# Optimization experiments

Measured on AMD Instinct MI355X. Metric: run time of the kernel, lower is better.

The kernel has to match this reference:

```python
import jax, jax.numpy as jnp
import numpy as np

B, L, DIM = 4, 8192, 512
HEADS, WIN = 8, 256
HID = int(DIM * 4.0)
HEAD_DIM = DIM // HEADS
EPS = 1e-5


def _layernorm(x, g, b):
    m = jnp.mean(x, axis=-1, keepdims=True)
    v = jnp.mean(jnp.square(x - m), axis=-1, keepdims=True)
    return (x - m) * jax.lax.rsqrt(v + EPS) * g + b


def setup_inputs() -> dict:
    key = jax.random.key(0)
    ks = jax.random.split(key, 8)
    s = 0.02
    return {
        "x": jax.random.normal(ks[0], (B, L, DIM), jnp.float32),
        "norm1_g": jnp.ones((DIM,), jnp.float32),
        "norm1_b": jnp.zeros((DIM,), jnp.float32),
        "qkv_w": jax.random.normal(ks[1], (DIM, 3 * DIM), jnp.float32) * s,
        "qkv_b": jnp.zeros((3 * DIM,), jnp.float32),
        "rpb_table": jax.random.normal(ks[2], (2 * WIN - 1, HEADS), jnp.float32) * s,
        "proj_w": jax.random.normal(ks[3], (DIM, DIM), jnp.float32) * s,
        "proj_b": jnp.zeros((DIM,), jnp.float32),
        "norm2_g": jnp.ones((DIM,), jnp.float32),
        "norm2_b": jnp.zeros((DIM,), jnp.float32),
        "fc1_w": jax.random.normal(ks[4], (DIM, HID), jnp.float32) * s,
        "fc1_b": jnp.zeros((HID,), jnp.float32),
        "fc2_w": jax.random.normal(ks[5], (HID, DIM), jnp.float32) * s,
        "fc2_b": jnp.zeros((DIM,), jnp.float32),
    }


def reference(x, norm1_g, norm1_b, qkv_w, qkv_b, rpb_table, proj_w, proj_b,
              norm2_g, norm2_b, fc1_w, fc1_b, fc2_w, fc2_b):
    scale = HEAD_DIM ** -0.5
    nW = L // WIN
    BW = B * nW

    shortcut = x
    h = _layernorm(x, norm1_g, norm1_b)
    xw = h.reshape(BW, WIN, DIM)

    qkv = (xw @ qkv_w + qkv_b).reshape(BW, WIN, 3, HEADS, HEAD_DIM)
    q = jnp.moveaxis(qkv[:, :, 0], 1, 2) * scale  # (BW, H, W, d)
    k = jnp.moveaxis(qkv[:, :, 1], 1, 2)
    v = jnp.moveaxis(qkv[:, :, 2], 1, 2)

    attn = jnp.einsum('bhqd,bhkd->bhqk', q, k)
    # relative position bias gather: (W, W, H) -> (H, W, W)
    coords = jnp.arange(WIN)
    ridx = coords[:, None] - coords[None, :] + WIN - 1
    bias = rpb_table[ridx]  # (W, W, H)
    attn = attn + jnp.transpose(bias, (2, 0, 1))[None]
    attn = jax.nn.softmax(attn, axis=-1)

    out = jnp.einsum('bhqk,bhkd->bhqd', attn, v)  # (BW, H, W, d)
    out = jnp.moveaxis(out, 1, 2).reshape(BW, WIN, DIM)
    out = out @ proj_w + proj_b

    x = shortcut + out.reshape(B, L, DIM)
    # NOTE: norm2 output feeds BOTH the residual branch and the MLP (as in source)
    x = _layernorm(x, norm2_g, norm2_b)
    m = jax.nn.gelu(x @ fc1_w + fc1_b, approximate=False) @ fc2_w + fc2_b
    return x + m
```

## Files before the change

kernel.cpp:

```cpp
#include <hip/hip_runtime.h>
#include <hip/hip_bf16.h>
#include <math.h>
#include <stdint.h>


typedef __attribute__((ext_vector_type(8))) __bf16 bf16x8;
typedef __attribute__((ext_vector_type(4))) __bf16 bf16x4;
typedef __attribute__((ext_vector_type(4))) float  f32x4;

#define NTOK  32768
#define DIMC  512
#define HEADS 8
#define WIN   256
#define HD    64
#define HIDC  2048

__device__ __forceinline__ void gld16(const __bf16* g, __bf16* l)
{
    __builtin_amdgcn_global_load_lds(
        (const __attribute__((address_space(1))) void*)g,
        (__attribute__((address_space(3))) void*)l, 16, 0, 0);
}

#define DSR(dst, base, off) \
    asm volatile("ds_read_b128 %0, %1 offset:" off : "=v"(dst) : "v"(base))

template<int MODE, int OUTF>
__global__ __launch_bounds__(512, 2) void gemm256(
    const __bf16* __restrict__ A, int lda,
    const __bf16* __restrict__ Bt, int ldb,
    const float* __restrict__ bias,
    const void* __restrict__ res, int res_f32,
    void* __restrict__ C, int ldc, int K,
    int nM, int nN)
{
    __shared__ __bf16 lds[2][2][16384];
    const int tid  = threadIdx.x;
    const int wave = tid >> 6, lane = tid & 63;
    const int quad = lane >> 4, l16 = lane & 15;
    const int wm = wave >> 2, wn = wave & 3;

    const int id  = blockIdx.x;
    const int xcd = id & 7;
    const int lid = id >> 3;
    const int mq  = lid / nN;
    const int mt  = xcd * (nM >> 3) + mq;
    const int nt  = lid - mq * nN;
    const int m0 = mt * 256, n0 = nt * 256;

    int aoff[4], boff[4];
    #pragma unroll
    for (int j = 0; j < 4; j++) {
        const int S = wave * 4 + j;
        const int row = (S >> 1) * 16 + l16;
        const int kof = (S & 1) * 32 + quad * 8;
        aoff[j] = (m0 + row) * lda + kof;
        boff[j] = (n0 + row) * ldb + kof;
    }

    const uint32_t lds0 =
        (uint32_t)(uintptr_t)(__attribute__((address_space(3))) void*)&lds[0][0][0];
    const uint32_t aAd0 = lds0 + wm * 16384 + lane * 16;
    const uint32_t bAd0 = lds0 + 32768 + wn * 8192 + lane * 16;

    f32x4 acc[8][4] = {};
    bf16x8 rA[4][2], rB[4][2];

    const int ntk = K >> 6;

    #pragma unroll
    for (int j = 0; j < 4; j++) {
        gld16(A  + aoff[j], &lds[0][0][(wave * 4 + j) * 512]);
        gld16(Bt + boff[j], &lds[0][1][(wave * 4 + j) * 512]);
    }
    #pragma unroll
    for (int j = 0; j < 4; j++) {
        gld16(A  + aoff[j] + 64, &lds[1][0][(wave * 4 + j) * 512]);
        gld16(Bt + boff[j] + 64, &lds[1][1][(wave * 4 + j) * 512]);
    }
    asm volatile("s_waitcnt vmcnt(8)");
    __builtin_amdgcn_s_barrier();

    for (int t = 0; t < ntk; ++t) {
        const int buf = t & 1;
        const uint32_t aAd = aAd0 + buf * 65536;
        const uint32_t bAd = bAd0 + buf * 65536;
        const bool pf = (t + 2 < ntk);
        const int kn = (t + 2) << 6;

        DSR(rA[0][0], aAd, "0");    DSR(rA[0][1], aAd, "1024");
        DSR(rA[1][0], aAd, "2048"); DSR(rA[1][1], aAd, "3072");
        DSR(rA[2][0], aAd, "4096"); DSR(rA[2][1], aAd, "5120");
        DSR(rA[3][0], aAd, "6144"); DSR(rA[3][1], aAd, "7168");
        DSR(rB[0][0], bAd, "0");    DSR(rB[0][1], bAd, "1024");
        DSR(rB[1][0], bAd, "2048"); DSR(rB[1][1], bAd, "3072");
        __builtin_amdgcn_s_barrier();
        asm volatile("s_waitcnt lgkmcnt(0)");
        __builtin_amdgcn_sched_barrier(0);
        __builtin_amdgcn_s_setprio(1);
        #pragma unroll
        for (int i = 0; i < 4; i++)
            #pragma unroll
            for (int j = 0; j < 2; j++)
                #pragma unroll
                for (int ks = 0; ks < 2; ks++)
                    acc[i][j] = __builtin_amdgcn_mfma_f32_16x16x32_bf16(
                        rB[j][ks], rA[i][ks], acc[i][j], 0, 0, 0);
        __builtin_amdgcn_s_setprio(0);
        __builtin_amdgcn_s_barrier();

        DSR(rB[2][0], bAd, "4096"); DSR(rB[2][1], bAd, "5120");
        DSR(rB[3][0], bAd, "6144"); DSR(rB[3][1], bAd, "7168");
        __builtin_amdgcn_s_barrier();
        asm volatile("s_waitcnt lgkmcnt(0)");
        __builtin_amdgcn_sched_barrier(0);
        __builtin_amdgcn_s_setprio(1);
        #pragma unroll
        for (int i = 0; i < 4; i++)
            #pragma unroll
            for (int j = 2; j < 4; j++)
                #pragma unroll
                for (int ks = 0; ks < 2; ks++)
                    acc[i][j] = __builtin_amdgcn_mfma_f32_16x16x32_bf16(
                        rB[j][ks], rA[i][ks], acc[i][j], 0, 0, 0);
        __builtin_amdgcn_s_setprio(0);
        __builtin_amdgcn_s_barrier();

        DSR(rA[0][0], aAd, "8192");  DSR(rA[0][1], aAd, "9216");
        DSR(rA[1][0], aAd, "10240"); DSR(rA[1][1], aAd, "11264");
        DSR(rA[2][0], aAd, "12288"); DSR(rA[2][1], aAd, "13312");
        DSR(rA[3][0], aAd, "14336"); DSR(rA[3][1], aAd, "15360");
        if (pf) {
            #pragma unroll
            for (int j = 0; j < 4; j++)
                gld16(Bt + boff[j] + kn, &lds[buf][1][(wave * 4 + j) * 512]);
        }
        __builtin_amdgcn_s_barrier();
        asm volatile("s_waitcnt lgkmcnt(0)");
        __builtin_amdgcn_sched_barrier(0);
        __builtin_amdgcn_s_setprio(1);
        #pragma unroll
        for (int i = 0; i < 4; i++)
            #pragma unroll
            for (int j = 0; j < 2; j++)
                #pragma unroll
                for (int ks = 0; ks < 2; ks++)
                    acc[4 + i][j] = __builtin_amdgcn_mfma_f32_16x16x32_bf16(
                        rB[j][ks], rA[i][ks], acc[4 + i][j], 0, 0, 0);
        __builtin_amdgcn_s_setprio(0);
        __builtin_amdgcn_s_barrier();

        if (pf) {
            #pragma unroll
            for (int j = 0; j < 4; j++)
                gld16(A + aoff[j] + kn, &lds[buf][0][(wave * 4 + j) * 512]);
        }
        __builtin_amdgcn_s_setprio(1);
        #pragma unroll
        for (int i = 0; i < 4; i++)
            #pragma unroll
            for (int j = 2; j < 4; j++)
                #pragma unroll
                for (int ks = 0; ks < 2; ks++)
                    acc[4 + i][j] = __builtin_amdgcn_mfma_f32_16x16x32_bf16(
                        rB[j][ks], rA[i][ks], acc[4 + i][j], 0, 0, 0);
        __builtin_amdgcn_s_setprio(0);
        if (pf)                  asm volatile("s_waitcnt vmcnt(8)");
        else if (t + 1 < ntk)    asm volatile("s_waitcnt vmcnt(0)");
        __builtin_amdgcn_s_barrier();
    }

    #pragma unroll
    for (int i = 0; i < 8; i++) {
        const int row = m0 + wm * 128 + i * 16 + l16;
        #pragma unroll
        for (int j = 0; j < 4; j++) {
            const int colb = n0 + wn * 64 + j * 16 + quad * 4;
            const size_t off = (size_t)row * ldc + colb;
            const f32x4 bv = *(const f32x4*)(bias + colb);
            f32x4 v;
            #pragma unroll
            for (int r = 0; r < 4; r++) v[r] = acc[i][j][r] + bv[r];
            if (MODE == 2) {
                #pragma unroll
                for (int r = 0; r < 4; r++)
                    v[r] = 0.5f * v[r] * (1.0f + erff(v[r] * 0.70710678118654752f));
            }
            if (MODE == 1) {
                if (res_f32) {
                    const f32x4 rv = *(const f32x4*)((const float*)res + off);
                    #pragma unroll
                    for (int r = 0; r < 4; r++) v[r] += rv[r];
                } else {
                    const bf16x4 rv = *(const bf16x4*)((const __bf16*)res + off);
                    #pragma unroll
                    for (int r = 0; r < 4; r++) v[r] += (float)rv[r];
                }
            }
            if (OUTF) {
                *(f32x4*)((float*)C + off) = v;
            } else {
                bf16x4 o;
                #pragma unroll
                for (int r = 0; r < 4; r++) o[r] = (__bf16)v[r];
                *(bf16x4*)((__bf16*)C + off) = o;
            }
        }
    }
}

__global__ __launch_bounds__(256) void attn_fused(
    const __bf16* __restrict__ qkvb, const float* __restrict__ rpb,
    const __bf16* __restrict__ Vt, __bf16* __restrict__ attnO)
{
    __shared__ __align__(16) __bf16 Ks[256 * 72];
    __shared__ float rpbs[320];
    const int bh = blockIdx.y;
    const int bw = bh >> 3, head = bh & 7;
    const int m0 = blockIdx.x * 64;
    const int tid = threadIdx.x;
    const __bf16* qb = qkvb + (size_t)bw * WIN * 1536 + head * HD;

    const int wave = tid >> 6, lane = tid & 63;
    const int quad = lane >> 4, l16 = lane & 15;

    bf16x8 af[2];
    #pragma unroll
    for (int ks = 0; ks < 2; ks++)
        af[ks] = *(const bf16x8*)(qb + (size_t)(m0 + wave * 16 + l16) * 1536
                                  + ks * 32 + quad * 8);

    {
        const int row = tid >> 3, l8 = (tid & 7) * 8;
        #pragma unroll
        for (int p = 0; p < 8; p++) {
            const int r = p * 32 + row;
            *(bf16x8*)(Ks + r * 72 + l8) =
                *(const bf16x8*)(qb + 512 + (size_t)r * 1536 + l8);
        }
        rpbs[tid] = rpb[(size_t)(m0 + tid) * HEADS + head];
        if (tid < 63) rpbs[256 + tid] = rpb[(size_t)(m0 + 256 + tid) * HEADS + head];
    }
    __syncthreads();

    f32x4 acc[16];
    #pragma unroll
    for (int nb = 0; nb < 16; nb++) acc[nb] = (f32x4){0.f, 0.f, 0.f, 0.f};
    #pragma unroll
    for (int nb = 0; nb < 16; nb++) {
        #pragma unroll
        for (int ks = 0; ks < 2; ks++) {
            bf16x8 bf = *(const bf16x8*)(Ks + (nb * 16 + l16) * 72 + ks * 32 + quad * 8);
            acc[nb] = __builtin_amdgcn_mfma_f32_16x16x32_bf16(bf, af[ks], acc[nb], 0, 0, 0);
        }
    }
    const int ql = wave * 16 + l16;
    #pragma unroll
    for (int nb = 0; nb < 16; nb++)
        #pragma unroll
        for (int r = 0; r < 4; r++)
            acc[nb][r] = acc[nb][r] * 0.125f
                       + rpbs[ql - (nb * 16 + quad * 4 + r) + 255];

    __syncthreads();

    char* Pb = (char*)Ks;
    {
        float m = -1e30f;
        #pragma unroll
        for (int nb = 0; nb < 16; nb++)
            #pragma unroll
            for (int r = 0; r < 4; r++) m = fmaxf(m, acc[nb][r]);
        m = fmaxf(m, __shfl_xor(m, 16));
        m = fmaxf(m, __shfl_xor(m, 32));
        float s = 0.f;
        #pragma unroll
        for (int nb = 0; nb < 16; nb++)
            #pragma unroll
            for (int r = 0; r < 4; r++) {
                acc[nb][r] = __expf(acc[nb][r] - m);
                s += acc[nb][r];
            }
        s += __shfl_xor(s, 16);
        s += __shfl_xor(s, 32);
        const float inv = 1.0f / s;
        const int rx = ql & 7;
        #pragma unroll
        for (int nb = 0; nb < 16; nb++) {
            bf16x4 o;
            #pragma unroll
            for (int r = 0; r < 4; r++) o[r] = (__bf16)(acc[nb][r] * inv);
            const int c = nb * 2 + (quad >> 1);
            *(bf16x4*)(Pb + ql * 512 + ((c ^ rx) << 4) + ((quad & 1) << 3)) = o;
        }
    }
    __syncthreads();

    const __bf16* Vtb = Vt + (size_t)bh * (HD * WIN);
    const int prow = wave * 16 + l16;
    const int px = prow & 7;
    f32x4 acc2[4] = {};
    #pragma unroll
    for (int ks2 = 0; ks2 < 8; ks2++) {
        const bf16x8 pa = *(const bf16x8*)(Pb + prow * 512
                                + (((ks2 * 4 + quad) ^ px) << 4));
        #pragma unroll
        for (int nb2 = 0; nb2 < 4; nb2++) {
            const bf16x8 vf = *(const bf16x8*)(Vtb + (size_t)(nb2 * 16 + l16) * WIN
                                + ks2 * 32 + quad * 8);
            acc2[nb2] = __builtin_amdgcn_mfma_f32_16x16x32_bf16(vf, pa, acc2[nb2], 0, 0, 0);
        }
    }
    {
        const int i = m0 + wave * 16 + l16;
        __bf16* ob = attnO + (size_t)(bw * WIN + i) * DIMC + head * HD;
        #pragma unroll
        for (int nb2 = 0; nb2 < 4; nb2++) {
            bf16x4 o;
            #pragma unroll
            for (int r = 0; r < 4; r++) o[r] = (__bf16)acc2[nb2][r];
            *(bf16x4*)(ob + nb2 * 16 + quad * 4) = o;
        }
    }
}

__global__ __launch_bounds__(256) void vtrans(
    const __bf16* __restrict__ qkvb, __bf16* __restrict__ Vt, int bh_base)
{
    __shared__ __align__(16) __bf16 s[WIN * 72];
    const int bh = bh_base + blockIdx.x;
    const int bw = bh >> 3, head = bh & 7;
    const int tid = threadIdx.x;
    const __bf16* V = qkvb + (size_t)bw * WIN * 1536 + 1024 + head * HD;
    #pragma unroll
    for (int it = 0; it < 8; it++) {
        int idx = it * 256 + tid;
        int j = idx >> 3;
        int d0 = (idx & 7) * 8;
        *(bf16x8*)(s + j * 72 + d0) = *(const bf16x8*)(V + (size_t)j * 1536 + d0);
    }
    __syncthreads();
    __bf16* out = Vt + (size_t)blockIdx.x * (HD * WIN);
    #pragma unroll
    for (int it = 0; it < 8; it++) {
        int idx = it * 256 + tid;
        int d  = idx >> 5;
        int j0 = (idx & 31) * 8;
        bf16x8 v;
        #pragma unroll
        for (int j = 0; j < 8; j++) v[j] = s[(j0 + j) * 72 + d];
        *(bf16x8*)(out + (size_t)d * WIN + j0) = v;
    }
}

__global__ __launch_bounds__(256) void ln_kernel(
    const void* X, int xf,
    const float* __restrict__ g, const float* __restrict__ b,
    __bf16* O)
{
    const int tok  = blockIdx.x * 4 + (threadIdx.x >> 6);
    const int lane = threadIdx.x & 63;
    const size_t base = (size_t)tok * DIMC + lane * 8;
    float v[8];
    if (xf) {
        const float* xp = (const float*)X + base;
        f32x4 a = *(const f32x4*)xp;
        f32x4 c = *(const f32x4*)(xp + 4);
        #pragma unroll
        for (int j = 0; j < 4; j++) { v[j] = a[j]; v[4 + j] = c[j]; }
    } else {
        bf16x8 xv = *(const bf16x8*)((const __bf16*)X + base);
        #pragma unroll
        for (int j = 0; j < 8; j++) v[j] = (float)xv[j];
    }
    float s = 0.f, s2 = 0.f;
    #pragma unroll
    for (int j = 0; j < 8; j++) { s += v[j]; s2 += v[j] * v[j]; }
    #pragma unroll
    for (int off = 32; off; off >>= 1) { s += __shfl_xor(s, off); s2 += __shfl_xor(s2, off); }
    const float mean = s * (1.0f / DIMC);
    const float var  = s2 * (1.0f / DIMC) - mean * mean;
    const float rstd = rsqrtf(var + 1e-5f);
    f32x4 ga = *(const f32x4*)(g + lane * 8);
    f32x4 gc = *(const f32x4*)(g + lane * 8 + 4);
    f32x4 ba = *(const f32x4*)(b + lane * 8);
    f32x4 bc = *(const f32x4*)(b + lane * 8 + 4);
    bf16x8 ov;
    #pragma unroll
    for (int j = 0; j < 4; j++) {
        ov[j]     = (__bf16)((v[j]     - mean) * rstd * ga[j] + ba[j]);
        ov[4 + j] = (__bf16)((v[4 + j] - mean) * rstd * gc[j] + bc[j]);
    }
    *(bf16x8*)(O + base) = ov;
}

__global__ __launch_bounds__(256) void wtrans(
    const float* __restrict__ W, __bf16* __restrict__ Wt, int K, int N)
{
    __shared__ __align__(16) __bf16 s[64 * 72];
    const int kb = blockIdx.y * 64, nb = blockIdx.x * 64;
    const int tid = threadIdx.x;
    #pragma unroll
    for (int it = 0; it < 2; it++) {
        int idx = it * 256 + tid;
        int lk = idx >> 3;
        int ln = (idx & 7) * 8;
        const float* wp = W + (size_t)(kb + lk) * N + nb + ln;
        f32x4 a = *(const f32x4*)wp;
        f32x4 c = *(const f32x4*)(wp + 4);
        bf16x8 v;
        #pragma unroll
        for (int j = 0; j < 4; j++) { v[j] = (__bf16)a[j]; v[4 + j] = (__bf16)c[j]; }
        *(bf16x8*)(s + lk * 72 + ln) = v;
    }
    __syncthreads();
    #pragma unroll
    for (int it = 0; it < 2; it++) {
        int idx = it * 256 + tid;
        int ln  = idx >> 3;
        int lkv = (idx & 7) * 8;
        bf16x8 v;
        #pragma unroll
        for (int j = 0; j < 8; j++) v[j] = s[(lkv + j) * 72 + ln];
        *(bf16x8*)(Wt + (size_t)(nb + ln) * K + kb + lkv) = v;
    }
}

extern "C" void kernel_launch(void* const* d_in, const int* in_sizes, int n_in,
                              void* d_out, int out_size, void* d_ws, size_t ws_size,
                              hipStream_t stream)
{
    const float* x      = (const float*)d_in[0];
    const float* n1g    = (const float*)d_in[1];
    const float* n1b    = (const float*)d_in[2];
    const float* qkv_w  = (const float*)d_in[3];
    const float* qkv_b  = (const float*)d_in[4];
    const float* rpb    = (const float*)d_in[5];
    const float* proj_w = (const float*)d_in[6];
    const float* proj_b = (const float*)d_in[7];
    const float* n2g    = (const float*)d_in[8];
    const float* n2b    = (const float*)d_in[9];
    const float* fc1_w  = (const float*)d_in[10];
    const float* fc1_b  = (const float*)d_in[11];
    const float* fc2_w  = (const float*)d_in[12];
    const float* fc2_b  = (const float*)d_in[13];
    float* out = (float*)d_out;

    char* ws = (char*)d_ws;
    __bf16* qkvb  = (__bf16*)(ws + 0);
    __bf16* hid   = (__bf16*)(ws + 0);
    __bf16* Vt    = (__bf16*)(ws + 100663296);
    __bf16* h     = (__bf16*)(ws + 134217728);
    __bf16* y     = h;
    __bf16* attnO = (__bf16*)(ws + 167772160);
    __bf16* wq_t  = (__bf16*)(ws + 209715200);
    __bf16* wp_t  = (__bf16*)(ws + 211288064);
    __bf16* w1_t  = (__bf16*)(ws + 211812352);
    __bf16* w2_t  = (__bf16*)(ws + 213909504);

    wtrans<<<dim3(1536 / 64, 512 / 64),  256, 0, stream>>>(qkv_w, wq_t, 512, 1536);
    wtrans<<<dim3(512 / 64,  512 / 64),  256, 0, stream>>>(proj_w, wp_t, 512, 512);
    wtrans<<<dim3(2048 / 64, 512 / 64),  256, 0, stream>>>(fc1_w, w1_t, 512, 2048);
    wtrans<<<dim3(512 / 64,  2048 / 64), 256, 0, stream>>>(fc2_w, w2_t, 2048, 512);

    ln_kernel<<<NTOK / 4, 256, 0, stream>>>(x, 1, n1g, n1b, h);

    gemm256<0, 0><<<768, 512, 0, stream>>>(
        h, DIMC, wq_t, DIMC, qkv_b, nullptr, 0, qkvb, 1536, DIMC, 128, 6);

    vtrans<<<1024, 256, 0, stream>>>(qkvb, Vt, 0);
    attn_fused<<<dim3(4, 1024), 256, 0, stream>>>(qkvb, rpb, Vt, attnO);

    gemm256<1, 0><<<256, 512, 0, stream>>>(
        attnO, DIMC, wp_t, DIMC, proj_b, x, 1, y, DIMC, DIMC, 128, 2);

    ln_kernel<<<NTOK / 4, 256, 0, stream>>>(y, 0, n2g, n2b, y);

    gemm256<2, 0><<<1024, 512, 0, stream>>>(
        y, DIMC, w1_t, DIMC, fc1_b, nullptr, 0, hid, HIDC, DIMC, 128, 8);

    gemm256<1, 1><<<256, 512, 0, stream>>>(
        hid, HIDC, w2_t, HIDC, fc2_b, y, 0, out, DIMC, HIDC, 128, 2);
}
```

Before: 634.0 us.

## Replace 256x256 double-buffered GEMM with 128x128 single-buffered 4-wave tile

```diff
diff --git a/kernel.cpp b/kernel.cpp
--- a/kernel.cpp
+++ b/kernel.cpp
@@ -26,7 +26,7 @@
     asm volatile("ds_read_b128 %0, %1 offset:" off : "=v"(dst) : "v"(base))
 
 template<int MODE, int OUTF>
-__global__ __launch_bounds__(512, 2) void gemm256(
+__global__ __launch_bounds__(256, 3) void gemm128m(
     const __bf16* __restrict__ A, int lda,
     const __bf16* __restrict__ Bt, int ldb,
     const float* __restrict__ bias,
@@ -34,11 +34,11 @@
     void* __restrict__ C, int ldc, int K,
     int nM, int nN)
 {
-    __shared__ __bf16 lds[2][2][16384];
+    __shared__ __bf16 lds[16384];
     const int tid  = threadIdx.x;
     const int wave = tid >> 6, lane = tid & 63;
     const int quad = lane >> 4, l16 = lane & 15;
-    const int wm = wave >> 2, wn = wave & 3;
+    const int wr = wave >> 1, wc = wave & 1;
 
     const int id  = blockIdx.x;
     const int xcd = id & 7;
@@ -46,7 +46,7 @@
     const int mq  = lid / nN;
     const int mt  = xcd * (nM >> 3) + mq;
     const int nt  = lid - mq * nN;
-    const int m0 = mt * 256, n0 = nt * 256;
+    const int m0 = mt * 128, n0 = nt * 128;
 
     int aoff[4], boff[4];
     #pragma unroll
@@ -59,123 +59,66 @@
     }
 
     const uint32_t lds0 =
-        (uint32_t)(uintptr_t)(__attribute__((address_space(3))) void*)&lds[0][0][0];
-    const uint32_t aAd0 = lds0 + wm * 16384 + lane * 16;
-    const uint32_t bAd0 = lds0 + 32768 + wn * 8192 + lane * 16;
-
-    f32x4 acc[8][4] = {};
+        (uint32_t)(uintptr_t)(__attribute__((address_space(3))) void*)&lds[0];
+    const uint32_t aAd = lds0 + wr * 8192 + lane * 16;
+    const uint32_t bAd = lds0 + 16384 + wc * 8192 + lane * 16;
+
+    f32x4 acc[4][4] = {};
     bf16x8 rA[4][2], rB[4][2];
 
     const int ntk = K >> 6;
 
     #pragma unroll
     for (int j = 0; j < 4; j++) {
-        gld16(A  + aoff[j], &lds[0][0][(wave * 4 + j) * 512]);
-        gld16(Bt + boff[j], &lds[0][1][(wave * 4 + j) * 512]);
-    }
-    #pragma unroll
-    for (int j = 0; j < 4; j++) {
-        gld16(A  + aoff[j] + 64, &lds[1][0][(wave * 4 + j) * 512]);
-        gld16(Bt + boff[j] + 64, &lds[1][1][(wave * 4 + j) * 512]);
-    }
-    asm volatile("s_waitcnt vmcnt(8)");
+        gld16(A  + aoff[j], &lds[(wave * 4 + j) * 512]);
+        gld16(Bt + boff[j], &lds[8192 + (wave * 4 + j) * 512]);
+    }
+    asm volatile("s_waitcnt vmcnt(0)");
     __builtin_amdgcn_s_barrier();
 
     for (int t = 0; t < ntk; ++t) {
-        const int buf = t & 1;
-        const uint32_t aAd = aAd0 + buf * 65536;
-        const uint32_t bAd = bAd0 + buf * 65536;
-        const bool pf = (t + 2 < ntk);
-        const int kn = (t + 2) << 6;
-
         DSR(rA[0][0], aAd, "0");    DSR(rA[0][1], aAd, "1024");
         DSR(rA[1][0], aAd, "2048"); DSR(rA[1][1], aAd, "3072");
         DSR(rA[2][0], aAd, "4096"); DSR(rA[2][1], aAd, "5120");
         DSR(rA[3][0], aAd, "6144"); DSR(rA[3][1], aAd, "7168");
         DSR(rB[0][0], bAd, "0");    DSR(rB[0][1], bAd, "1024");
         DSR(rB[1][0], bAd, "2048"); DSR(rB[1][1], bAd, "3072");
-        __builtin_amdgcn_s_barrier();
+        DSR(rB[2][0], bAd, "4096"); DSR(rB[2][1], bAd, "5120");
+        DSR(rB[3][0], bAd, "6144"); DSR(rB[3][1], bAd, "7168");
         asm volatile("s_waitcnt lgkmcnt(0)");
         __builtin_amdgcn_sched_barrier(0);
+        __builtin_amdgcn_s_barrier();
+
+        const bool pf = (t + 1 < ntk);
+        if (pf) {
+            const int kn = (t + 1) << 6;
+            #pragma unroll
+            for (int j = 0; j < 4; j++) {
+                gld16(A  + aoff[j] + kn, &lds[(wave * 4 + j) * 512]);
+                gld16(Bt + boff[j] + kn, &lds[8192 + (wave * 4 + j) * 512]);
+            }
+        }
+
         __builtin_amdgcn_s_setprio(1);
         #pragma unroll
         for (int i = 0; i < 4; i++)
             #pragma unroll
-            for (int j = 0; j < 2; j++)
+            for (int j = 0; j < 4; j++)
                 #pragma unroll
                 for (int ks = 0; ks < 2; ks++)
                     acc[i][j] = __builtin_amdgcn_mfma_f32_16x16x32_bf16(
                         rB[j][ks], rA[i][ks], acc[i][j], 0, 0, 0);
         __builtin_amdgcn_s_setprio(0);
+        if (pf) asm volatile("s_waitcnt vmcnt(0)");
         __builtin_amdgcn_s_barrier();
-
-        DSR(rB[2][0], bAd, "4096"); DSR(rB[2][1], bAd, "5120");
-        DSR(rB[3][0], bAd, "6144"); DSR(rB[3][1], bAd, "7168");
-        __builtin_amdgcn_s_barrier();
-        asm volatile("s_waitcnt lgkmcnt(0)");
-        __builtin_amdgcn_sched_barrier(0);
-        __builtin_amdgcn_s_setprio(1);
-        #pragma unroll
-        for (int i = 0; i < 4; i++)
-            #pragma unroll
-            for (int j = 2; j < 4; j++)
-                #pragma unroll
-                for (int ks = 0; ks < 2; ks++)
-                    acc[i][j] = __builtin_amdgcn_mfma_f32_16x16x32_bf16(
-                        rB[j][ks], rA[i][ks], acc[i][j], 0, 0, 0);
-        __builtin_amdgcn_s_setprio(0);
-        __builtin_amdgcn_s_barrier();
-
-        DSR(rA[0][0], aAd, "8192");  DSR(rA[0][1], aAd, "9216");
-        DSR(rA[1][0], aAd, "10240"); DSR(rA[1][1], aAd, "11264");
-        DSR(rA[2][0], aAd, "12288"); DSR(rA[2][1], aAd, "13312");
-        DSR(rA[3][0], aAd, "14336"); DSR(rA[3][1], aAd, "15360");
-        if (pf) {
-            #pragma unroll
-            for (int j = 0; j < 4; j++)
-                gld16(Bt + boff[j] + kn, &lds[buf][1][(wave * 4 + j) * 512]);
-        }
-        __builtin_amdgcn_s_barrier();
-        asm volatile("s_waitcnt lgkmcnt(0)");
-        __builtin_amdgcn_sched_barrier(0);
-        __builtin_amdgcn_s_setprio(1);
-        #pragma unroll
-        for (int i = 0; i < 4; i++)
-            #pragma unroll
-            for (int j = 0; j < 2; j++)
-                #pragma unroll
-                for (int ks = 0; ks < 2; ks++)
-                    acc[4 + i][j] = __builtin_amdgcn_mfma_f32_16x16x32_bf16(
-                        rB[j][ks], rA[i][ks], acc[4 + i][j], 0, 0, 0);
-        __builtin_amdgcn_s_setprio(0);
-        __builtin_amdgcn_s_barrier();
-
-        if (pf) {
-            #pragma unroll
-            for (int j = 0; j < 4; j++)
-                gld16(A + aoff[j] + kn, &lds[buf][0][(wave * 4 + j) * 512]);
-        }
-        __builtin_amdgcn_s_setprio(1);
-        #pragma unroll
-        for (int i = 0; i < 4; i++)
-            #pragma unroll
-            for (int j = 2; j < 4; j++)
-                #pragma unroll
-                for (int ks = 0; ks < 2; ks++)
-                    acc[4 + i][j] = __builtin_amdgcn_mfma_f32_16x16x32_bf16(
-                        rB[j][ks], rA[i][ks], acc[4 + i][j], 0, 0, 0);
-        __builtin_amdgcn_s_setprio(0);
-        if (pf)                  asm volatile("s_waitcnt vmcnt(8)");
-        else if (t + 1 < ntk)    asm volatile("s_waitcnt vmcnt(0)");
-        __builtin_amdgcn_s_barrier();
-    }
-
-    #pragma unroll
-    for (int i = 0; i < 8; i++) {
-        const int row = m0 + wm * 128 + i * 16 + l16;
+    }
+
+    #pragma unroll
+    for (int i = 0; i < 4; i++) {
+        const int row = m0 + wr * 64 + i * 16 + l16;
         #pragma unroll
         for (int j = 0; j < 4; j++) {
-            const int colb = n0 + wn * 64 + j * 16 + quad * 4;
+            const int colb = n0 + wc * 64 + j * 16 + quad * 4;
             const size_t off = (size_t)row * ldc + colb;
             const f32x4 bv = *(const f32x4*)(bias + colb);
             f32x4 v;
@@ -465,20 +408,20 @@
 
     ln_kernel<<<NTOK / 4, 256, 0, stream>>>(x, 1, n1g, n1b, h);
 
-    gemm256<0, 0><<<768, 512, 0, stream>>>(
-        h, DIMC, wq_t, DIMC, qkv_b, nullptr, 0, qkvb, 1536, DIMC, 128, 6);
+    gemm128m<0, 0><<<3072, 256, 0, stream>>>(
+        h, DIMC, wq_t, DIMC, qkv_b, nullptr, 0, qkvb, 1536, DIMC, 256, 12);
 
     vtrans<<<1024, 256, 0, stream>>>(qkvb, Vt, 0);
     attn_fused<<<dim3(4, 1024), 256, 0, stream>>>(qkvb, rpb, Vt, attnO);
 
-    gemm256<1, 0><<<256, 512, 0, stream>>>(
-        attnO, DIMC, wp_t, DIMC, proj_b, x, 1, y, DIMC, DIMC, 128, 2);
+    gemm128m<1, 0><<<1024, 256, 0, stream>>>(
+        attnO, DIMC, wp_t, DIMC, proj_b, x, 1, y, DIMC, DIMC, 256, 4);
 
     ln_kernel<<<NTOK / 4, 256, 0, stream>>>(y, 0, n2g, n2b, y);
 
-    gemm256<2, 0><<<1024, 512, 0, stream>>>(
-        y, DIMC, w1_t, DIMC, fc1_b, nullptr, 0, hid, HIDC, DIMC, 128, 8);
-
-    gemm256<1, 1><<<256, 512, 0, stream>>>(
-        hid, HIDC, w2_t, HIDC, fc2_b, y, 0, out, DIMC, HIDC, 128, 2);
-}
+    gemm128m<2, 0><<<4096, 256, 0, stream>>>(
+        y, DIMC, w1_t, DIMC, fc1_b, nullptr, 0, hid, HIDC, DIMC, 256, 16);
+
+    gemm128m<1, 1><<<1024, 256, 0, stream>>>(
+        hid, HIDC, w2_t, HIDC, fc2_b, y, 0, out, DIMC, HIDC, 256, 4);
+}
```

New measurement: 746.2 us. +17.7%, slower.
